# Kernel optimization log

Hardware: AMD Instinct MI355X
Metric: run time of the kernel (lower is better)

The kernel has to match this reference:

```python
import jax, jax.numpy as jnp
import numpy as np

N = 100000      # nodes
E = 1600000     # directed edges (avg degree 16)
F_IN = 128
HID = 64
OUT = 10


def setup_inputs() -> dict:
    key = jax.random.key(0)
    ks = jax.random.split(key, 6)
    x = jax.random.normal(ks[0], (N, F_IN), dtype=jnp.float32)
    edge_index = jax.random.randint(ks[1], (2, E), 0, N, dtype=jnp.int32)
    # Glorot-scaled weights like PyG's GCNConv.lin; bias added post-aggregation
    W1 = jax.random.normal(ks[2], (F_IN, HID), dtype=jnp.float32) * np.float32(1.0 / np.sqrt(F_IN))
    b1 = jnp.zeros((HID,), dtype=jnp.float32)
    W2 = jax.random.normal(ks[3], (HID, OUT), dtype=jnp.float32) * np.float32(1.0 / np.sqrt(HID))
    b2 = jnp.zeros((OUT,), dtype=jnp.float32)
    return {"x": x, "edge_index": edge_index, "W1": W1, "b1": b1, "W2": W2, "b2": b2}


def _gcn_norm(edge_index, num_nodes):
    """Add self-loops and compute symmetric normalization D^-1/2 A D^-1/2 (PyG gcn_norm)."""
    loops = jnp.arange(num_nodes, dtype=edge_index.dtype)
    src = jnp.concatenate([edge_index[0], loops])
    dst = jnp.concatenate([edge_index[1], loops])
    deg = jax.ops.segment_sum(jnp.ones_like(dst, dtype=jnp.float32), dst, num_segments=num_nodes)
    dinv = jnp.where(deg > 0, jax.lax.rsqrt(deg), 0.0)  # inf -> 0 as in PyG
    norm = dinv[src] * dinv[dst]  # [E+N]
    return src, dst, norm


def _gcn_conv(x, src, dst, norm, W, b, num_nodes):
    h = x @ W                                   # transform first (smaller dim aggregated)
    msg = h[src] * norm[:, None]                # gather + scale
    agg = jax.ops.segment_sum(msg, dst, num_segments=num_nodes)  # scatter-add
    return agg + b


def reference(x, edge_index, W1, b1, W2, b2):
    src, dst, norm = _gcn_norm(edge_index, N)
    h = jax.nn.relu(_gcn_conv(x, src, dst, norm, W1, b1, N))
    # F.dropout(training=self.training): identity in eval mode
    out = _gcn_conv(h, src, dst, norm, W2, b2, N)
    return out
```

## Files before the change

### kernel.cpp

```cpp
#include <hip/hip_runtime.h>
#include <hip/hip_fp16.h>

static constexpr int F = 128;
static constexpr int H = 64;
static constexpr int O = 10;
static constexpr int PS = 12;
static constexpr int NBUK_MAX = 256;
static constexpr int CAP = 12288;
static constexpr int EPB = 4096;
static constexpr int XPAD = 136;

typedef _Float16 half8 __attribute__((ext_vector_type(8)));
typedef float floatx4 __attribute__((ext_vector_type(4)));

__global__ __launch_bounds__(256) void k_init(int* __restrict__ bcntg,
                                              int* __restrict__ cnt, int n,
                                              const float* __restrict__ W1,
                                              __half* __restrict__ W1f) {
    int b = blockIdx.x, t = threadIdx.x;
    if (b == 0) {
        bcntg[t] = 0;
        if (t == 0) cnt[n] = 0;
    } else {
        int i = (b - 1) * 256 + t;
        int j = i & 7, lane = (i >> 3) & 63, sc = i >> 9;
        int s = sc >> 2, c = sc & 3;
        int k = s * 32 + (lane >> 4) * 8 + j;
        int nn = c * 16 + (lane & 15);
        W1f[i] = __float2half(W1[k * H + nn]);
    }
}

__global__ __launch_bounds__(256) void k_bin(const int* __restrict__ src,
                                             const int* __restrict__ dst,
                                             int* __restrict__ bcntg,
                                             unsigned* __restrict__ ebuf, int e_total) {
    __shared__ int hist[NBUK_MAX];
    __shared__ int base[NBUK_MAX];
    __shared__ int loc[NBUK_MAX];
    int t = threadIdx.x;
    hist[t] = 0;
    loc[t] = 0;
    __syncthreads();
    int i0 = blockIdx.x * EPB;
    int i1 = min(i0 + EPB, e_total);
    int i = i0 + 4 * t;
    for (; i + 3 < i1; i += 1024) {
        int4 d4 = *(const int4*)&dst[i];
        atomicAdd(&hist[d4.x >> 9], 1);
        atomicAdd(&hist[d4.y >> 9], 1);
        atomicAdd(&hist[d4.z >> 9], 1);
        atomicAdd(&hist[d4.w >> 9], 1);
    }
    for (; i < i1; ++i) atomicAdd(&hist[dst[i] >> 9], 1);
    __syncthreads();
    if (hist[t] > 0) base[t] = atomicAdd(&bcntg[t], hist[t]);
    __syncthreads();
    i = i0 + 4 * t;
    for (; i + 3 < i1; i += 1024) {
        int4 s4 = *(const int4*)&src[i];
        int4 d4 = *(const int4*)&dst[i];
#pragma unroll
        for (int u = 0; u < 4; ++u) {
            int s = (&s4.x)[u], d = (&d4.x)[u];
            int b = d >> 9;
            int r = base[b] + atomicAdd(&loc[b], 1);
            if (r < CAP)
                ebuf[(size_t)b * CAP + r] = ((unsigned)(d & 511) << 17) | (unsigned)s;
        }
    }
    for (; i < i1; ++i) {
        int s = src[i], d = dst[i];
        int b = d >> 9;
        int r = base[b] + atomicAdd(&loc[b], 1);
        if (r < CAP)
            ebuf[(size_t)b * CAP + r] = ((unsigned)(d & 511) << 17) | (unsigned)s;
    }
}

__global__ __launch_bounds__(256) void k_bcount(const unsigned* __restrict__ ebuf,
                                                const int* __restrict__ bcntg,
                                                int* __restrict__ cnt,
                                                float* __restrict__ dinv, int n_nodes) {
    __shared__ int hc[512];
    int t = threadIdx.x, b = blockIdx.x, n0 = b << 9;
    hc[t] = 0;
    hc[t + 256] = 0;
    __syncthreads();
    int cb = bcntg[b];
    const unsigned* eb = ebuf + (size_t)b * CAP;
    int i = 4 * t;
    for (; i + 3 < cb; i += 1024) {
        uint4 e4 = *(const uint4*)&eb[i];
        atomicAdd(&hc[e4.x >> 17], 1);
        atomicAdd(&hc[e4.y >> 17], 1);
        atomicAdd(&hc[e4.z >> 17], 1);
        atomicAdd(&hc[e4.w >> 17], 1);
    }
    for (; i < cb; ++i) atomicAdd(&hc[eb[i] >> 17], 1);
    __syncthreads();
#pragma unroll
    for (int u = 0; u < 2; ++u) {
        int n = n0 + t + u * 256;
        if (n < n_nodes) {
            int c = hc[t + u * 256];
            cnt[n] = c;
            dinv[n] = rsqrtf((float)c + 1.0f);
        }
    }
}

__global__ __launch_bounds__(256) void k_scan1(const int* __restrict__ cnt,
                                               int* __restrict__ rowptr,
                                               int* __restrict__ bsum, int n) {
    __shared__ int s[256];
    int t = threadIdx.x;
    int i = blockIdx.x * 256 + t;
    int v = (i < n) ? cnt[i] : 0;
    s[t] = v;
    __syncthreads();
    for (int off = 1; off < 256; off <<= 1) {
        int x = (t >= off) ? s[t - off] : 0;
        __syncthreads();
        s[t] += x;
        __syncthreads();
    }
    if (i < n) rowptr[i] = s[t] - v;
    if (t == 255) bsum[blockIdx.x] = s[255];
}

__global__ __launch_bounds__(512) void k_scan2(int* __restrict__ bsum, int nb) {
    __shared__ int s[512];
    int t = threadIdx.x;
    int v = (t < nb) ? bsum[t] : 0;
    s[t] = v;
    __syncthreads();
    for (int off = 1; off < 512; off <<= 1) {
        int x = (t >= off) ? s[t - off] : 0;
        __syncthreads();
        s[t] += x;
        __syncthreads();
    }
    if (t < nb) bsum[t] = s[t] - v;
}

__global__ __launch_bounds__(256) void k_scan3(int* __restrict__ rowptr,
                                               const int* __restrict__ bsum, int n) {
    int i = blockIdx.x * 256 + threadIdx.x;
    if (i < n) rowptr[i] += bsum[blockIdx.x];
}

__global__ __launch_bounds__(256) void k_fillb(const unsigned* __restrict__ ebuf,
                                               const int* __restrict__ bcntg,
                                               const int* __restrict__ rowptr,
                                               int* __restrict__ esrc, int n_nodes) {
    __shared__ int curs[512];
    int t = threadIdx.x, b = blockIdx.x, n0 = b << 9;
#pragma unroll
    for (int u = 0; u < 2; ++u) {
        int n = n0 + t + u * 256;
        if (n < n_nodes) curs[t + u * 256] = rowptr[n];
    }
    __syncthreads();
    int cb = bcntg[b];
    const unsigned* eb = ebuf + (size_t)b * CAP;
    int i = 4 * t;
    for (; i + 3 < cb; i += 1024) {
        uint4 e4 = *(const uint4*)&eb[i];
#pragma unroll
        for (int u = 0; u < 4; ++u) {
            unsigned e = (&e4.x)[u];
            int r = atomicAdd(&curs[e >> 17], 1);
            esrc[r] = (int)(e & 0x1FFFFu);
        }
    }
    for (; i < cb; ++i) {
        unsigned e = eb[i];
        int r = atomicAdd(&curs[e >> 17], 1);
        esrc[r] = (int)(e & 0x1FFFFu);
    }
}

__global__ __launch_bounds__(256, 4) void k_gemm1(
    const float* __restrict__ x, const __half* __restrict__ W1f,
    const float* __restrict__ dinv, __half* __restrict__ y, int n_nodes) {
    __shared__ __half xh[64 * XPAD];
    const int tid = threadIdx.x;
    const int lane = tid & 63;
    const int w = tid >> 6;
    const int row0 = blockIdx.x * 64;

    half8 bf[16];
    const uint4* wf = (const uint4*)W1f;
#pragma unroll
    for (int sc = 0; sc < 16; ++sc) {
        union { uint4 u; half8 h; } tmp;
        tmp.u = wf[sc * 64 + lane];
        bf[sc] = tmp.h;
    }

    for (int i = tid; i < 64 * 32; i += 256) {
        int r = i >> 5, k4 = i & 31;
        int gr = row0 + r;
        if (gr < n_nodes) {
            float4 v = *(const float4*)&x[(size_t)gr * F + 4 * k4];
            __half2 p0 = __floats2half2_rn(v.x, v.y);
            __half2 p1 = __floats2half2_rn(v.z, v.w);
            uint2 pk = make_uint2(*(unsigned*)&p0, *(unsigned*)&p1);
            *(uint2*)&xh[r * XPAD + 4 * k4] = pk;
        }
    }
    __syncthreads();

    const int m16 = lane & 15, quad = lane >> 4;
    floatx4 acc[4];
#pragma unroll
    for (int c = 0; c < 4; ++c) acc[c] = (floatx4){0.f, 0.f, 0.f, 0.f};
#pragma unroll
    for (int s = 0; s < 4; ++s) {
        union { uint4 u; half8 h; } ua;
        ua.u = *(const uint4*)&xh[(16 * w + m16) * XPAD + s * 32 + quad * 8];
#pragma unroll
        for (int c = 0; c < 4; ++c)
            acc[c] = __builtin_amdgcn_mfma_f32_16x16x32_f16(ua.h, bf[s * 4 + c],
                                                            acc[c], 0, 0, 0);
    }
#pragma unroll
    for (int r = 0; r < 4; ++r) {
        int grow = row0 + 16 * w + quad * 4 + r;
        if (grow < n_nodes) {
            float d = dinv[grow];
#pragma unroll
            for (int c = 0; c < 4; ++c)
                y[(size_t)grow * H + c * 16 + m16] = __float2half(acc[c][r] * d);
        }
    }
}

__global__ __launch_bounds__(256) void k_gather1(
    const uint2* __restrict__ yq, const int* __restrict__ rowptr,
    const int* __restrict__ esrc, const float* __restrict__ dinv,
    const float* __restrict__ b1, uint2* __restrict__ hq, int n_nodes) {
    const int l = threadIdx.x & 63;
    const int g = l >> 4;
    const int c = l & 15;
    const int n = blockIdx.x * 4 + (threadIdx.x >> 6);
    if (n >= n_nodes) return;
    const int beg = rowptr[n], end = rowptr[n + 1];
    const int deg = end - beg;
    int idx = (l < deg) ? esrc[beg + l] : 0;
    float2 aA = make_float2(0.f, 0.f);
    float2 aB = make_float2(0.f, 0.f);
    if (g == 0) {
        uint2 v = yq[(size_t)n * 16 + c];
        float2 fA = __half22float2(*(const __half2*)&v.x);
        float2 fB = __half22float2(*(const __half2*)&v.y);
        aA.x += fA.x; aA.y += fA.y; aB.x += fB.x; aB.y += fB.y;
    }
    const int dlim = min(deg, 64);
    int k = 0;
    for (; k + 15 < dlim; k += 16) {
#pragma unroll
        for (int u = 0; u < 4; ++u) {
            int s = __shfl(idx, k + 4 * u + g, 64);
            uint2 v = yq[(size_t)s * 16 + c];
            float2 fA = __half22float2(*(const __half2*)&v.x);
            float2 fB = __half22float2(*(const __half2*)&v.y);
            aA.x += fA.x; aA.y += fA.y; aB.x += fB.x; aB.y += fB.y;
        }
    }
    for (; k < dlim; k += 4) {
        int slot = k + g;
        int s = __shfl(idx, min(slot, dlim - 1), 64);
        if (slot < dlim) {
            uint2 v = yq[(size_t)s * 16 + c];
            float2 fA = __half22float2(*(const __half2*)&v.x);
            float2 fB = __half22float2(*(const __half2*)&v.y);
            aA.x += fA.x; aA.y += fA.y; aB.x += fB.x; aB.y += fB.y;
        }
    }
    for (int kk = 64 + g; kk < deg; kk += 4) {
        int s = esrc[beg + kk];
        uint2 v = yq[(size_t)s * 16 + c];
        float2 fA = __half22float2(*(const __half2*)&v.x);
        float2 fB = __half22float2(*(const __half2*)&v.y);
        aA.x += fA.x; aA.y += fA.y; aB.x += fB.x; aB.y += fB.y;
    }
#pragma unroll
    for (int off = 16; off <= 32; off <<= 1) {
        aA.x += __shfl_xor(aA.x, off, 64);
        aA.y += __shfl_xor(aA.y, off, 64);
        aB.x += __shfl_xor(aB.x, off, 64);
        aB.y += __shfl_xor(aB.y, off, 64);
    }
    if (g == 0) {
        float4 bb = ((const float4*)b1)[c];
        float d = dinv[n];
        float h0 = fmaxf(fmaf(d, aA.x, bb.x), 0.0f);
        float h1 = fmaxf(fmaf(d, aA.y, bb.y), 0.0f);
        float h2 = fmaxf(fmaf(d, aB.x, bb.z), 0.0f);
        float h3 = fmaxf(fmaf(d, aB.y, bb.w), 0.0f);
        __half2 p0 = __floats2half2_rn(h0, h1);
        __half2 p1 = __floats2half2_rn(h2, h3);
        hq[(size_t)n * 16 + c] = make_uint2(*(const unsigned*)&p0, *(const unsigned*)&p1);
    }
}

__global__ __launch_bounds__(256) void k_zs(
    const __half* __restrict__ h, const float* __restrict__ W2,
    const float* __restrict__ dinv, unsigned* __restrict__ zs_u, int n_nodes) {
    __shared__ unsigned zbuf[256 * (PS / 2)];
    const int t = threadIdx.x;
    const int n0 = blockIdx.x * 256;
    const int n = n0 + t;
    if (n < n_nodes) {
        float acc[O];
#pragma unroll
        for (int j = 0; j < O; ++j) acc[j] = 0.f;
        const __half2* hr = (const __half2*)(h + (size_t)n * H);
#pragma unroll
        for (int k2 = 0; k2 < H / 2; ++k2) {
            float2 hv = __half22float2(hr[k2]);
#pragma unroll
            for (int j = 0; j < O; ++j) {
                acc[j] = fmaf(hv.x, W2[(2 * k2 + 0) * O + j], acc[j]);
                acc[j] = fmaf(hv.y, W2[(2 * k2 + 1) * O + j], acc[j]);
            }
        }
        float d = dinv[n];
#pragma unroll
        for (int q = 0; q < O / 2; ++q) {
            __half2 p = __floats2half2_rn(acc[2 * q] * d, acc[2 * q + 1] * d);
            zbuf[t * (PS / 2) + q] = *(const unsigned*)&p;
        }
        zbuf[t * (PS / 2) + 5] = 0u;
    }
    __syncthreads();
    int total = (min(n0 + 256, n_nodes) - n0) * (PS / 2);
    unsigned* zo = zs_u + (size_t)n0 * (PS / 2);
    for (int i = t; i < total; i += 256) zo[i] = zbuf[i];
}

__global__ __launch_bounds__(256) void k_gather2(
    const unsigned* __restrict__ zs_u, const int* __restrict__ rowptr,
    const int* __restrict__ esrc, const float* __restrict__ dinv,
    const float* __restrict__ b2, float* __restrict__ out, int n_nodes) {
    const int l = threadIdx.x & 63;
    const int j = l & 7;
    const int sbase = l & ~7;
    const int n = blockIdx.x * 32 + (threadIdx.x >> 3);
    if (n >= n_nodes) return;
    const int beg = rowptr[n], end = rowptr[n + 1];
    const int deg = end - beg;
    float2 acc = make_float2(0.f, 0.f);
    if (j < 5) {
        unsigned v = zs_u[(size_t)n * (PS / 2) + j];
        acc = __half22float2(*(const __half2*)&v);
    }
    for (int k0 = 0; k0 < deg; k0 += 8) {
        int idx = (k0 + j < deg) ? esrc[beg + k0 + j] : 0;
        int m = min(8, deg - k0);
        for (int e = 0; e < m; ++e) {
            int s = __shfl(idx, sbase + e, 64);
            if (j < 5) {
                unsigned v = zs_u[(size_t)s * (PS / 2) + j];
                float2 f = __half22float2(*(const __half2*)&v);
                acc.x += f.x;
                acc.y += f.y;
            }
        }
    }
    if (j < 5) {
        float2 bb = ((const float2*)b2)[j];
        float d = dinv[n];
        float2 o = make_float2(fmaf(d, acc.x, bb.x), fmaf(d, acc.y, bb.y));
        *(float2*)&out[(size_t)n * O + 2 * j] = o;
    }
}

extern "C" void kernel_launch(void* const* d_in, const int* in_sizes, int n_in,
                              void* d_out, int out_size, void* d_ws, size_t ws_size,
                              hipStream_t stream) {
    const float* x  = (const float*)d_in[0];
    const int*   ei = (const int*)d_in[1];
    const float* W1 = (const float*)d_in[2];
    const float* b1 = (const float*)d_in[3];
    const float* W2 = (const float*)d_in[4];
    const float* b2 = (const float*)d_in[5];
    float* out = (float*)d_out;

    const int N = in_sizes[0] / F;
    const int E = in_sizes[1] / 2;
    const int* src = ei;
    const int* dst = ei + E;

    float* yr   = (float*)d_ws;
    float* hr   = yr + (size_t)N * H;
    __half* y   = (__half*)yr;
    __half* h   = (__half*)hr;
    unsigned* ebuf = (unsigned*)hr;
    __half* W1f = (__half*)(hr + (size_t)N * H - F * H);
    float* zr   = hr + (size_t)N * H;
    unsigned* zs_u = (unsigned*)zr;
    float* dinv = zr + (size_t)N * O;
    int* cnt    = (int*)(dinv + N);
    int* rowptr = cnt + (N + 1);
    int* bsum   = rowptr + (N + 1);
    int* bcntg  = bsum + 512;
    int* esrc   = bcntg + 256;

    const int NBUK   = (N + 511) >> 9;
    const int nb_n1  = (N + 256) / 256;
    const int nb_bin = (E + EPB - 1) / EPB;

    k_init<<<1 + F * H / 256, 256, 0, stream>>>(bcntg, cnt, N, W1, W1f);
    k_bin<<<nb_bin, 256, 0, stream>>>(src, dst, bcntg, ebuf, E);
    k_bcount<<<NBUK, 256, 0, stream>>>(ebuf, bcntg, cnt, dinv, N);
    k_scan1<<<nb_n1, 256, 0, stream>>>(cnt, rowptr, bsum, N + 1);
    k_scan2<<<1, 512, 0, stream>>>(bsum, nb_n1);
    k_scan3<<<nb_n1, 256, 0, stream>>>(rowptr, bsum, N + 1);
    k_fillb<<<NBUK, 256, 0, stream>>>(ebuf, bcntg, rowptr, esrc, N);
    k_gemm1<<<(N + 63) / 64, 256, 0, stream>>>(x, W1f, dinv, y, N);
    k_gather1<<<(N + 3) / 4, 256, 0, stream>>>((const uint2*)y, rowptr, esrc,
                                               dinv, b1, (uint2*)h, N);
    k_zs<<<(N + 255) / 256, 256, 0, stream>>>(h, W2, dinv, zs_u, N);
    k_gather2<<<(N + 31) / 32, 256, 0, stream>>>(zs_u, rowptr, esrc, dinv, b2, out, N);
}
```

Measured before the change: 220.0 us.

## Fuse CSR build into per-bucket sort with padded rows and sentinel node

Replaces the count, three-pass global scan and fill kernels with a single per-bucket kernel that does a local scan and writes esrc into a fixed-capacity region per bucket. Each row's edge count is rounded up to a multiple of 16, and the padding slots point to a zeroed sentinel node N. This lets the gather kernels drop their tail loops and bounds checks. It removes four launches and the global scan, at the cost of extra padded gathers that read the zero row and a risk of overflowing ESCAP when a bucket is highly skewed.

```diff
diff --git a/kernel.cpp b/kernel.cpp
--- a/kernel.cpp
+++ b/kernel.cpp
@@ -4,9 +4,10 @@
 static constexpr int F = 128;
 static constexpr int H = 64;
 static constexpr int O = 10;
-static constexpr int PS = 12;
+static constexpr int PSU = 6;
 static constexpr int NBUK_MAX = 256;
 static constexpr int CAP = 12288;
+static constexpr int ESCAP = 14336;
 static constexpr int EPB = 4096;
 static constexpr int XPAD = 136;
 
@@ -14,13 +15,15 @@
 typedef float floatx4 __attribute__((ext_vector_type(4)));
 
 __global__ __launch_bounds__(256) void k_init(int* __restrict__ bcntg,
-                                              int* __restrict__ cnt, int n,
                                               const float* __restrict__ W1,
-                                              __half* __restrict__ W1f) {
+                                              __half* __restrict__ W1f,
+                                              unsigned* __restrict__ yN,
+                                              unsigned* __restrict__ zsN) {
     int b = blockIdx.x, t = threadIdx.x;
     if (b == 0) {
         bcntg[t] = 0;
-        if (t == 0) cnt[n] = 0;
+        if (t < 32) yN[t] = 0u;
+        if (t < PSU) zsN[t] = 0u;
     } else {
         int i = (b - 1) * 256 + t;
         int j = i & 7, lane = (i >> 3) & 63, sc = i >> 9;
@@ -78,16 +81,18 @@
     }
 }
 
-__global__ __launch_bounds__(256) void k_bcount(const unsigned* __restrict__ ebuf,
-                                                const int* __restrict__ bcntg,
-                                                int* __restrict__ cnt,
-                                                float* __restrict__ dinv, int n_nodes) {
+__global__ __launch_bounds__(256) void k_bsort(
+    const unsigned* __restrict__ ebuf, const int* __restrict__ bcntg,
+    int* __restrict__ rowbeg, int* __restrict__ degp, float* __restrict__ dinv,
+    int* __restrict__ esrc, int n_nodes) {
     __shared__ int hc[512];
+    __shared__ int sa[512];
+    __shared__ int sb[512];
     int t = threadIdx.x, b = blockIdx.x, n0 = b << 9;
     hc[t] = 0;
     hc[t + 256] = 0;
     __syncthreads();
-    int cb = bcntg[b];
+    int cb = min(bcntg[b], CAP);
     const unsigned* eb = ebuf + (size_t)b * CAP;
     int i = 4 * t;
     for (; i + 3 < cb; i += 1024) {
@@ -101,83 +106,60 @@
     __syncthreads();
 #pragma unroll
     for (int u = 0; u < 2; ++u) {
-        int n = n0 + t + u * 256;
+        int ii = t + 256 * u;
+        sa[ii] = (hc[ii] + 15) & ~15;
+    }
+    __syncthreads();
+    int* A = sa;
+    int* Bp = sb;
+    for (int off = 1; off < 512; off <<= 1) {
+#pragma unroll
+        for (int u = 0; u < 2; ++u) {
+            int ii = t + 256 * u;
+            int v = A[ii];
+            if (ii >= off) v += A[ii - off];
+            Bp[ii] = v;
+        }
+        __syncthreads();
+        int* tmp = A; A = Bp; Bp = tmp;
+    }
+#pragma unroll
+    for (int u = 0; u < 2; ++u) {
+        int ii = t + 256 * u;
+        int cnt = hc[ii];
+        int cp = (cnt + 15) & ~15;
+        int excl = A[ii] - cp;
+        Bp[ii] = excl;
+        int n = n0 + ii;
         if (n < n_nodes) {
-            int c = hc[t + u * 256];
-            cnt[n] = c;
-            dinv[n] = rsqrtf((float)c + 1.0f);
-        }
-    }
-}
-
-__global__ __launch_bounds__(256) void k_scan1(const int* __restrict__ cnt,
-                                               int* __restrict__ rowptr,
-                                               int* __restrict__ bsum, int n) {
-    __shared__ int s[256];
-    int t = threadIdx.x;
-    int i = blockIdx.x * 256 + t;
-    int v = (i < n) ? cnt[i] : 0;
-    s[t] = v;
-    __syncthreads();
-    for (int off = 1; off < 256; off <<= 1) {
-        int x = (t >= off) ? s[t - off] : 0;
-        __syncthreads();
-        s[t] += x;
-        __syncthreads();
-    }
-    if (i < n) rowptr[i] = s[t] - v;
-    if (t == 255) bsum[blockIdx.x] = s[255];
-}
-
-__global__ __launch_bounds__(512) void k_scan2(int* __restrict__ bsum, int nb) {
-    __shared__ int s[512];
-    int t = threadIdx.x;
-    int v = (t < nb) ? bsum[t] : 0;
-    s[t] = v;
-    __syncthreads();
-    for (int off = 1; off < 512; off <<= 1) {
-        int x = (t >= off) ? s[t - off] : 0;
-        __syncthreads();
-        s[t] += x;
-        __syncthreads();
-    }
-    if (t < nb) bsum[t] = s[t] - v;
-}
-
-__global__ __launch_bounds__(256) void k_scan3(int* __restrict__ rowptr,
-                                               const int* __restrict__ bsum, int n) {
-    int i = blockIdx.x * 256 + threadIdx.x;
-    if (i < n) rowptr[i] += bsum[blockIdx.x];
-}
-
-__global__ __launch_bounds__(256) void k_fillb(const unsigned* __restrict__ ebuf,
-                                               const int* __restrict__ bcntg,
-                                               const int* __restrict__ rowptr,
-                                               int* __restrict__ esrc, int n_nodes) {
-    __shared__ int curs[512];
-    int t = threadIdx.x, b = blockIdx.x, n0 = b << 9;
-#pragma unroll
-    for (int u = 0; u < 2; ++u) {
-        int n = n0 + t + u * 256;
-        if (n < n_nodes) curs[t + u * 256] = rowptr[n];
-    }
-    __syncthreads();
-    int cb = bcntg[b];
-    const unsigned* eb = ebuf + (size_t)b * CAP;
-    int i = 4 * t;
+            rowbeg[n] = b * ESCAP + excl;
+            degp[n] = cp;
+            dinv[n] = rsqrtf((float)cnt + 1.0f);
+        }
+    }
+    __syncthreads();
+    int* es = esrc + (size_t)b * ESCAP;
+    i = 4 * t;
     for (; i + 3 < cb; i += 1024) {
         uint4 e4 = *(const uint4*)&eb[i];
 #pragma unroll
         for (int u = 0; u < 4; ++u) {
             unsigned e = (&e4.x)[u];
-            int r = atomicAdd(&curs[e >> 17], 1);
-            esrc[r] = (int)(e & 0x1FFFFu);
+            int r = atomicAdd(&Bp[e >> 17], 1);
+            es[r] = (int)(e & 0x1FFFFu);
         }
     }
     for (; i < cb; ++i) {
         unsigned e = eb[i];
-        int r = atomicAdd(&curs[e >> 17], 1);
-        esrc[r] = (int)(e & 0x1FFFFu);
+        int r = atomicAdd(&Bp[e >> 17], 1);
+        es[r] = (int)(e & 0x1FFFFu);
+    }
+    __syncthreads();
+#pragma unroll
+    for (int u = 0; u < 2; ++u) {
+        int ii = t + 256 * u;
+        int end = A[ii];
+        for (int p = Bp[ii]; p < end; ++p) es[p] = n_nodes;
     }
 }
 
@@ -238,17 +220,18 @@
 }
 
 __global__ __launch_bounds__(256) void k_gather1(
-    const uint2* __restrict__ yq, const int* __restrict__ rowptr,
-    const int* __restrict__ esrc, const float* __restrict__ dinv,
-    const float* __restrict__ b1, uint2* __restrict__ hq, int n_nodes) {
+    const uint2* __restrict__ yq, const int* __restrict__ rowbeg,
+    const int* __restrict__ degp, const int* __restrict__ esrc,
+    const float* __restrict__ dinv, const float* __restrict__ b1,
+    uint2* __restrict__ hq, int n_nodes) {
     const int l = threadIdx.x & 63;
     const int g = l >> 4;
     const int c = l & 15;
     const int n = blockIdx.x * 4 + (threadIdx.x >> 6);
     if (n >= n_nodes) return;
-    const int beg = rowptr[n], end = rowptr[n + 1];
-    const int deg = end - beg;
-    int idx = (l < deg) ? esrc[beg + l] : 0;
+    const int beg = rowbeg[n];
+    const int dp = degp[n];
+    const int idx = esrc[beg + l];
     float2 aA = make_float2(0.f, 0.f);
     float2 aB = make_float2(0.f, 0.f);
     if (g == 0) {
@@ -257,9 +240,8 @@
         float2 fB = __half22float2(*(const __half2*)&v.y);
         aA.x += fA.x; aA.y += fA.y; aB.x += fB.x; aB.y += fB.y;
     }
-    const int dlim = min(deg, 64);
-    int k = 0;
-    for (; k + 15 < dlim; k += 16) {
+    const int dlim = min(dp, 64);
+    for (int k = 0; k < dlim; k += 16) {
 #pragma unroll
         for (int u = 0; u < 4; ++u) {
             int s = __shfl(idx, k + 4 * u + g, 64);
@@ -269,18 +251,8 @@
             aA.x += fA.x; aA.y += fA.y; aB.x += fB.x; aB.y += fB.y;
         }
     }
-    for (; k < dlim; k += 4) {
-        int slot = k + g;
-        int s = __shfl(idx, min(slot, dlim - 1), 64);
-        if (slot < dlim) {
-            uint2 v = yq[(size_t)s * 16 + c];
-            float2 fA = __half22float2(*(const __half2*)&v.x);
-            float2 fB = __half22float2(*(const __half2*)&v.y);
-            aA.x += fA.x; aA.y += fA.y; aB.x += fB.x; aB.y += fB.y;
-        }
-    }
-    for (int kk = 64 + g; kk < deg; kk += 4) {
-        int s = esrc[beg + kk];
+    for (int kk = 64; kk < dp; kk += 4) {
+        int s = esrc[beg + kk + g];
         uint2 v = yq[(size_t)s * 16 + c];
         float2 fA = __half22float2(*(const __half2*)&v.x);
         float2 fB = __half22float2(*(const __half2*)&v.y);
@@ -309,7 +281,7 @@
 __global__ __launch_bounds__(256) void k_zs(
     const __half* __restrict__ h, const float* __restrict__ W2,
     const float* __restrict__ dinv, unsigned* __restrict__ zs_u, int n_nodes) {
-    __shared__ unsigned zbuf[256 * (PS / 2)];
+    __shared__ unsigned zbuf[256 * PSU];
     const int t = threadIdx.x;
     const int n0 = blockIdx.x * 256;
     const int n = n0 + t;
@@ -331,43 +303,40 @@
 #pragma unroll
         for (int q = 0; q < O / 2; ++q) {
             __half2 p = __floats2half2_rn(acc[2 * q] * d, acc[2 * q + 1] * d);
-            zbuf[t * (PS / 2) + q] = *(const unsigned*)&p;
-        }
-        zbuf[t * (PS / 2) + 5] = 0u;
-    }
-    __syncthreads();
-    int total = (min(n0 + 256, n_nodes) - n0) * (PS / 2);
-    unsigned* zo = zs_u + (size_t)n0 * (PS / 2);
+            zbuf[t * PSU + q] = *(const unsigned*)&p;
+        }
+        zbuf[t * PSU + 5] = 0u;
+    }
+    __syncthreads();
+    int total = (min(n0 + 256, n_nodes) - n0) * PSU;
+    unsigned* zo = zs_u + (size_t)n0 * PSU;
     for (int i = t; i < total; i += 256) zo[i] = zbuf[i];
 }
 
 __global__ __launch_bounds__(256) void k_gather2(
-    const unsigned* __restrict__ zs_u, const int* __restrict__ rowptr,
-    const int* __restrict__ esrc, const float* __restrict__ dinv,
-    const float* __restrict__ b2, float* __restrict__ out, int n_nodes) {
+    const unsigned* __restrict__ zs_u, const int* __restrict__ rowbeg,
+    const int* __restrict__ degp, const int* __restrict__ esrc,
+    const float* __restrict__ dinv, const float* __restrict__ b2,
+    float* __restrict__ out, int n_nodes) {
     const int l = threadIdx.x & 63;
     const int j = l & 7;
     const int sbase = l & ~7;
+    const int jj = (j < 5) ? j : 5;
     const int n = blockIdx.x * 32 + (threadIdx.x >> 3);
     if (n >= n_nodes) return;
-    const int beg = rowptr[n], end = rowptr[n + 1];
-    const int deg = end - beg;
-    float2 acc = make_float2(0.f, 0.f);
-    if (j < 5) {
-        unsigned v = zs_u[(size_t)n * (PS / 2) + j];
-        acc = __half22float2(*(const __half2*)&v);
-    }
-    for (int k0 = 0; k0 < deg; k0 += 8) {
-        int idx = (k0 + j < deg) ? esrc[beg + k0 + j] : 0;
-        int m = min(8, deg - k0);
-        for (int e = 0; e < m; ++e) {
+    const int beg = rowbeg[n];
+    const int dp = degp[n];
+    unsigned v0 = zs_u[(size_t)n * PSU + jj];
+    float2 acc = __half22float2(*(const __half2*)&v0);
+    for (int k0 = 0; k0 < dp; k0 += 8) {
+        int idx = esrc[beg + k0 + j];
+#pragma unroll
+        for (int e = 0; e < 8; ++e) {
             int s = __shfl(idx, sbase + e, 64);
-            if (j < 5) {
-                unsigned v = zs_u[(size_t)s * (PS / 2) + j];
-                float2 f = __half22float2(*(const __half2*)&v);
-                acc.x += f.x;
-                acc.y += f.y;
-            }
+            unsigned v = zs_u[(size_t)s * PSU + jj];
+            float2 f = __half22float2(*(const __half2*)&v);
+            acc.x += f.x;
+            acc.y += f.y;
         }
     }
     if (j < 5) {
@@ -377,6 +346,8 @@
         *(float2*)&out[(size_t)n * O + 2 * j] = o;
     }
 }
+
+static inline size_t align256(size_t v) { return (v + 255) & ~(size_t)255; }
 
 extern "C" void kernel_launch(void* const* d_in, const int* in_sizes, int n_in,
                               void* d_out, int out_size, void* d_ws, size_t ws_size,
@@ -393,36 +364,36 @@
     const int E = in_sizes[1] / 2;
     const int* src = ei;
     const int* dst = ei + E;
-
-    float* yr   = (float*)d_ws;
-    float* hr   = yr + (size_t)N * H;
-    __half* y   = (__half*)yr;
-    __half* h   = (__half*)hr;
-    unsigned* ebuf = (unsigned*)hr;
-    __half* W1f = (__half*)(hr + (size_t)N * H - F * H);
-    float* zr   = hr + (size_t)N * H;
-    unsigned* zs_u = (unsigned*)zr;
-    float* dinv = zr + (size_t)N * O;
-    int* cnt    = (int*)(dinv + N);
-    int* rowptr = cnt + (N + 1);
-    int* bsum   = rowptr + (N + 1);
-    int* bcntg  = bsum + 512;
-    int* esrc   = bcntg + 256;
-
-    const int NBUK   = (N + 511) >> 9;
-    const int nb_n1  = (N + 256) / 256;
+    const int NBUK = (N + 511) >> 9;
+
+    char* base = (char*)d_ws;
+    __half* y = (__half*)base;
+    size_t ysz = align256((size_t)(N + 1) * H * 2);
+    char* hreg = base + ysz;
+    __half* h = (__half*)hreg;
+    unsigned* ebuf = (unsigned*)hreg;
+    __half* W1f = (__half*)(hreg + (size_t)N * H * 2 - (size_t)F * H * 2);
+    size_t hsz = align256((size_t)N * H * 2);
+    char* zreg = hreg + hsz;
+    unsigned* zs_u = (unsigned*)zreg;
+    size_t zsz = align256((size_t)(N + 1) * PSU * 4);
+    float* dinv = (float*)(zreg + zsz);
+    int* rowbeg = (int*)(dinv + N);
+    int* degp = rowbeg + N;
+    int* bcntg = degp + N;
+    int* esrc = bcntg + 256;
+
     const int nb_bin = (E + EPB - 1) / EPB;
 
-    k_init<<<1 + F * H / 256, 256, 0, stream>>>(bcntg, cnt, N, W1, W1f);
+    k_init<<<1 + F * H / 256, 256, 0, stream>>>(bcntg, W1, W1f,
+                                                (unsigned*)(y + (size_t)N * H),
+                                                zs_u + (size_t)N * PSU);
     k_bin<<<nb_bin, 256, 0, stream>>>(src, dst, bcntg, ebuf, E);
-    k_bcount<<<NBUK, 256, 0, stream>>>(ebuf, bcntg, cnt, dinv, N);
-    k_scan1<<<nb_n1, 256, 0, stream>>>(cnt, rowptr, bsum, N + 1);
-    k_scan2<<<1, 512, 0, stream>>>(bsum, nb_n1);
-    k_scan3<<<nb_n1, 256, 0, stream>>>(rowptr, bsum, N + 1);
-    k_fillb<<<NBUK, 256, 0, stream>>>(ebuf, bcntg, rowptr, esrc, N);
+    k_bsort<<<NBUK, 256, 0, stream>>>(ebuf, bcntg, rowbeg, degp, dinv, esrc, N);
     k_gemm1<<<(N + 63) / 64, 256, 0, stream>>>(x, W1f, dinv, y, N);
-    k_gather1<<<(N + 3) / 4, 256, 0, stream>>>((const uint2*)y, rowptr, esrc,
-                                               dinv, b1, (uint2*)h, N);
+    k_gather1<<<(N + 3) / 4, 256, 0, stream>>>((const uint2*)y, rowbeg, degp,
+                                               esrc, dinv, b1, (uint2*)h, N);
     k_zs<<<(N + 255) / 256, 256, 0, stream>>>(h, W2, dinv, zs_u, N);
-    k_gather2<<<(N + 31) / 32, 256, 0, stream>>>(zs_u, rowptr, esrc, dinv, b2, out, N);
-}
+    k_gather2<<<(N + 31) / 32, 256, 0, stream>>>(zs_u, rowbeg, degp, esrc,
+                                                 dinv, b2, out, N);
+}
```

Result: faster. 199.9 us (-9.1%).
